# Performance work log

Hardware: AMD Instinct MI355X
Metric: run time of the kernel (lower is better)

The kernel has to match this reference:

```python
import jax, jax.numpy as jnp
import numpy as np

T, IN, HID, OUT, B = 256, 1024, 1024, 1024, 128


def setup_inputs() -> dict:
    key = jax.random.key(0)
    k1, k2, k3, k4 = jax.random.split(key, 4)
    return {
        "inputs": jax.random.normal(k1, (T, IN, B), dtype=jnp.float32),
        "h_prev": jnp.zeros((HID, B), dtype=jnp.float32),
        "Wxh": jax.random.normal(k2, (HID, IN), dtype=jnp.float32) * 0.01,
        "Whh": jax.random.normal(k3, (HID, HID), dtype=jnp.float32) * 0.01,
        "Why": jax.random.normal(k4, (OUT, HID), dtype=jnp.float32) * 0.01,
        "bh": jnp.zeros((HID, 1), dtype=jnp.float32),
        "by": jnp.zeros((OUT, 1), dtype=jnp.float32),
    }


def reference(inputs, h_prev, Wxh, Whh, Why, bh, by):
    # inputs: [T, IN, B]; h: [HID, B]
    def step(h, x):
        h = jnp.tanh(Wxh @ x + Whh @ h + bh)
        y = Why @ h + by
        return h, y

    h_final, ys = jax.lax.scan(step, h_prev, inputs)
    return ys, h_final  # ys: [T, OUT, B], h_final: [HID, B]
```

## Files before the change

kernel.cpp:

```cpp
#include <hip/hip_runtime.h>
#include <cmath>

#define T_STEPS 256
#define DIN  1024
#define DHID 1024
#define DOUT 1024
#define NB   128
#define BH   (DHID*NB)

typedef unsigned short u16;
typedef unsigned int   u32;
typedef unsigned long long u64;
typedef __attribute__((ext_vector_type(8))) __bf16 bf16x8;
typedef __attribute__((ext_vector_type(4))) float  f32x4;

__device__ __forceinline__ u16 f2bf(float f){
  u32 u = __builtin_bit_cast(u32, f);
  u32 r = (u + 0x7fffu + ((u >> 16) & 1u)) >> 16;
  return (u16)r;
}
__device__ __forceinline__ float bf2f(u16 h){
  u32 u = ((u32)h) << 16;
  return __builtin_bit_cast(float, u);
}

__device__ __forceinline__ u64 ld_agent_u64(const u64* p){
  return __hip_atomic_load(p, __ATOMIC_RELAXED, __HIP_MEMORY_SCOPE_AGENT);
}
__device__ __forceinline__ void st_agent_u64(u64* p, u64 v){
  __hip_atomic_store(p, v, __ATOMIC_RELAXED, __HIP_MEMORY_SCOPE_AGENT);
}

__global__ __launch_bounds__(256) void wconv(const float* __restrict__ w0,
                                             const float* __restrict__ w1,
                                             const float* __restrict__ w2,
                                             u16* __restrict__ dst){
  const int idx = blockIdx.x*256 + threadIdx.x;
  const int seg = idx >> 18;
  const int off = idx & 262143;
  const float* src = seg==0 ? w0 : (seg==1 ? w1 : w2);
  const float4 v = ((const float4*)src)[off];
  ushort4 o = make_ushort4(f2bf(v.x), f2bf(v.y), f2bf(v.z), f2bf(v.w));
  ((ushort4*)dst)[idx] = o;
}

__global__ __launch_bounds__(256) void hprevT(const float* __restrict__ hp,
                                              u16* __restrict__ HT0){
  const int tid = blockIdx.x*256 + threadIdx.x;
  const int b = tid >> 10, m = tid & 1023;
  HT0[tid] = f2bf(hp[(size_t)m*NB + b]);
}

__global__ __launch_bounds__(256) void xT_k(const float* __restrict__ x,
                                            u16* __restrict__ xt){
  __shared__ float tile[64][65];
  const int t  = blockIdx.z;
  const int k0 = blockIdx.y*64;
  const int b0 = blockIdx.x*64;
  const int tx = threadIdx.x & 63, ty = threadIdx.x >> 6;
  const float* src = x + (size_t)t*DIN*NB + (size_t)k0*NB + b0;
#pragma unroll
  for(int r=0;r<16;r++){ int k = r*4 + ty; tile[k][tx] = src[(size_t)k*NB + tx]; }
  __syncthreads();
  u16* dst = xt + (size_t)t*NB*DIN + (size_t)b0*DIN + k0;
#pragma unroll
  for(int r=0;r<16;r++){ int b = r*4 + ty; dst[(size_t)b*DIN + tx] = f2bf(tile[tx][b]); }
}

__global__ __launch_bounds__(256) void gemm_xw(const u16* __restrict__ XT,
                                               const u16* __restrict__ WxB,
                                               const float* __restrict__ bh,
                                               u16* __restrict__ AT){
  const int t  = blockIdx.y;
  const int mj = blockIdx.x;
  __shared__ __align__(16) u16 As[128*40];
  __shared__ __align__(16) u16 Bs[128*40];
  const u16* aG = XT + (size_t)t*NB*DIN;
  const u16* bG = WxB + (size_t)mj*128*DIN;
  const int tid = threadIdx.x;
  const int lane = tid & 63, w = tid >> 6;
  const int wr = (w & 1)*64, wc = (w >> 1)*64;
  const int l15 = lane & 15, q = lane >> 4;
  const int sr = tid >> 2;
  const int sk = (tid & 3)*8;

  f32x4 acc[4][4] = {};
  uint4 pa0 = *(const uint4*)&aG[(size_t)sr*DIN + sk];
  uint4 pa1 = *(const uint4*)&aG[(size_t)(sr+64)*DIN + sk];
  uint4 pb0 = *(const uint4*)&bG[(size_t)sr*DIN + sk];
  uint4 pb1 = *(const uint4*)&bG[(size_t)(sr+64)*DIN + sk];

  for(int it = 0; it < DIN/32; ++it){
    __syncthreads();
    *(uint4*)&As[sr*40 + sk]      = pa0;
    *(uint4*)&As[(sr+64)*40 + sk] = pa1;
    *(uint4*)&Bs[sr*40 + sk]      = pb0;
    *(uint4*)&Bs[(sr+64)*40 + sk] = pb1;
    __syncthreads();
    if(it < DIN/32 - 1){
      const int k0 = (it+1)*32;
      pa0 = *(const uint4*)&aG[(size_t)sr*DIN + k0 + sk];
      pa1 = *(const uint4*)&aG[(size_t)(sr+64)*DIN + k0 + sk];
      pb0 = *(const uint4*)&bG[(size_t)sr*DIN + k0 + sk];
      pb1 = *(const uint4*)&bG[(size_t)(sr+64)*DIN + k0 + sk];
    }
    bf16x8 af[4], bf[4];
#pragma unroll
    for(int i=0;i<4;i++) af[i] = *(const bf16x8*)&As[(wr + i*16 + l15)*40 + q*8];
#pragma unroll
    for(int j=0;j<4;j++) bf[j] = *(const bf16x8*)&Bs[(wc + j*16 + l15)*40 + q*8];
#pragma unroll
    for(int i=0;i<4;i++)
#pragma unroll
      for(int j=0;j<4;j++)
        acc[i][j] = __builtin_amdgcn_mfma_f32_16x16x32_bf16(af[i], bf[j], acc[i][j], 0,0,0);
  }

  u16* out = AT + (size_t)t*NB*DHID;
#pragma unroll
  for(int j=0;j<4;j++){
    const int mg = mj*128 + wc + j*16 + l15;
    const float bhv = bh[mg];
#pragma unroll
    for(int i=0;i<4;i++){
#pragma unroll
      for(int r=0;r<4;r++){
        const int bg = wr + i*16 + q*4 + r;
        out[(size_t)bg*DHID + mg] = f2bf(acc[i][j][r] + bhv);
      }
    }
  }
}

#define RSTEP_BLOCKS 64
__global__ __launch_bounds__(256, 1) void rnn_steps(const u16* __restrict__ WhB,
                                                    const u16* __restrict__ AT,
                                                    u16* __restrict__ HT,
                                                    u32* __restrict__ flags){
  const int mslice = blockIdx.x & 7;
  const int bg     = blockIdx.x >> 3;
  __shared__ __align__(16) u16 Hs[16*1032];
  __shared__ __align__(16) u16 Es[4*16*40];
  const int tid = threadIdx.x;
  const int lane = tid & 63, w = tid >> 6;
  const int l15 = lane & 15, q = lane >> 4, q8 = q*8;
  const int mw = mslice*128 + w*32;

  bf16x8 wf0[32], wf1[32];
  { const u16* ws0 = WhB + (size_t)(mw + l15)*DHID;
    const u16* ws1 = WhB + (size_t)(mw + 16 + l15)*DHID;
#pragma unroll
    for(int i=0;i<32;i++){ wf0[i] = *(const bf16x8*)&ws0[i*32 + q8];
                           wf1[i] = *(const bf16x8*)&ws1[i*32 + q8]; }
  }

  const int hr = tid >> 4;
  const int hc = tid & 15;
  const int eb = lane >> 2, ec = lane & 3;

  for(int t=0; t<T_STEPS; ++t){
    const u64* Hp64 = (const u64*)(HT + (size_t)t*BH + (size_t)(bg*16 + hr)*DHID) + hc;

    u64 hv[16];
#pragma unroll
    for(int i=0;i<16;i++) hv[i] = ld_agent_u64(Hp64 + i*16);

    const u16* At = AT + (size_t)t*BH;
    u16 aval[2][4];
#pragma unroll
    for(int h=0;h<2;h++)
#pragma unroll
      for(int r=0;r<4;r++)
        aval[h][r] = At[(size_t)(bg*16 + q*4 + r)*DHID + mw + h*16 + l15];

    u64* hs64 = (u64*)&Hs[hr*1032] + hc;
#pragma unroll
    for(int i=0;i<16;i++) hs64[i*16] = hv[i];
    __syncthreads();

    f32x4 a0e = {0,0,0,0}, a0o = {0,0,0,0}, a1e = {0,0,0,0}, a1o = {0,0,0,0};
#pragma unroll
    for(int kk=0;kk<32;kk+=2){
      bf16x8 ae = *(const bf16x8*)&Hs[l15*1032 + kk*32 + q8];
      bf16x8 ao = *(const bf16x8*)&Hs[l15*1032 + (kk+1)*32 + q8];
      a0e = __builtin_amdgcn_mfma_f32_16x16x32_bf16(ae, wf0[kk],   a0e, 0,0,0);
      a1e = __builtin_amdgcn_mfma_f32_16x16x32_bf16(ae, wf1[kk],   a1e, 0,0,0);
      a0o = __builtin_amdgcn_mfma_f32_16x16x32_bf16(ao, wf0[kk+1], a0o, 0,0,0);
      a1o = __builtin_amdgcn_mfma_f32_16x16x32_bf16(ao, wf1[kk+1], a1o, 0,0,0);
    }
    f32x4 acc0 = a0e + a0o, acc1 = a1e + a1o;

    u16* Ew = Es + w*640;
#pragma unroll
    for(int r=0;r<4;r++){
      float v0 = acc0[r] + bf2f(aval[0][r]);
      float v1 = acc1[r] + bf2f(aval[1][r]);
      Ew[(q*4+r)*40 + l15]      = f2bf(tanhf(v0));
      Ew[(q*4+r)*40 + 16 + l15] = f2bf(tanhf(v1));
    }
    __syncthreads();
    u64 h0 = *(const u64*)&Ew[eb*40 + ec*8];
    u64 h1 = *(const u64*)&Ew[eb*40 + ec*8 + 4];
    u64* Hn = (u64*)(HT + (size_t)(t+1)*BH + (size_t)(bg*16 + eb)*DHID + mw + ec*8);
    st_agent_u64(Hn,     h0);
    st_agent_u64(Hn + 1, h1);

    asm volatile("s_waitcnt vmcnt(0)" ::: "memory");

    if(t < T_STEPS-1){
      __syncthreads();
      if(tid == 0)
        __hip_atomic_store(&flags[(size_t)(bg*8 + mslice)*32], (u32)(t+1),
                           __ATOMIC_RELAXED, __HIP_MEMORY_SCOPE_AGENT);
      if(tid < 8){
        while(__hip_atomic_load(&flags[(size_t)(bg*8 + tid)*32],
                                __ATOMIC_RELAXED, __HIP_MEMORY_SCOPE_AGENT) < (u32)(t+1))
          ;
      }
      __syncthreads();
    }
  }
}

__global__ __launch_bounds__(256) void gemm_hy(const u16* __restrict__ WyB,
                                               const u16* __restrict__ HT,
                                               const float* __restrict__ by,
                                               float* __restrict__ Y){
  const int t  = blockIdx.y;
  const int mi = blockIdx.x;
  __shared__ __align__(16) u16 As[128*40];
  __shared__ __align__(16) u16 Bs[128*40];
  const u16* aG = WyB + (size_t)mi*128*DHID;
  const u16* bG = HT  + (size_t)(t+1)*BH;
  const int tid = threadIdx.x;
  const int lane = tid & 63, w = tid >> 6;
  const int wr = (w & 1)*64, wc = (w >> 1)*64;
  const int l15 = lane & 15, q = lane >> 4;
  const int sr = tid >> 2;
  const int sk = (tid & 3)*8;

  f32x4 acc[4][4] = {};
  uint4 pa0 = *(const uint4*)&aG[(size_t)sr*DHID + sk];
  uint4 pa1 = *(const uint4*)&aG[(size_t)(sr+64)*DHID + sk];
  uint4 pb0 = *(const uint4*)&bG[(size_t)sr*DHID + sk];
  uint4 pb1 = *(const uint4*)&bG[(size_t)(sr+64)*DHID + sk];

  for(int it = 0; it < DHID/32; ++it){
    __syncthreads();
    *(uint4*)&As[sr*40 + sk]      = pa0;
    *(uint4*)&As[(sr+64)*40 + sk] = pa1;
    *(uint4*)&Bs[sr*40 + sk]      = pb0;
    *(uint4*)&Bs[(sr+64)*40 + sk] = pb1;
    __syncthreads();
    if(it < DHID/32 - 1){
      const int k0 = (it+1)*32;
      pa0 = *(const uint4*)&aG[(size_t)sr*DHID + k0 + sk];
      pa1 = *(const uint4*)&aG[(size_t)(sr+64)*DHID + k0 + sk];
      pb0 = *(const uint4*)&bG[(size_t)sr*DHID + k0 + sk];
      pb1 = *(const uint4*)&bG[(size_t)(sr+64)*DHID + k0 + sk];
    }
    bf16x8 af[4], bf[4];
#pragma unroll
    for(int i=0;i<4;i++) af[i] = *(const bf16x8*)&As[(wr + i*16 + l15)*40 + q*8];
#pragma unroll
    for(int j=0;j<4;j++) bf[j] = *(const bf16x8*)&Bs[(wc + j*16 + l15)*40 + q*8];
#pragma unroll
    for(int i=0;i<4;i++)
#pragma unroll
      for(int j=0;j<4;j++)
        acc[i][j] = __builtin_amdgcn_mfma_f32_16x16x32_bf16(af[i], bf[j], acc[i][j], 0,0,0);
  }

  float* out = Y + (size_t)t*DOUT*NB;
#pragma unroll
  for(int i=0;i<4;i++){
#pragma unroll
    for(int r=0;r<4;r++){
      const int og = mi*128 + wr + i*16 + q*4 + r;
      const float byv = by[og];
#pragma unroll
      for(int j=0;j<4;j++){
        const int bg = wc + j*16 + l15;
        out[(size_t)og*NB + bg] = acc[i][j][r] + byv;
      }
    }
  }
}

__global__ __launch_bounds__(256) void hfinal(const u16* __restrict__ HT,
                                              float* __restrict__ dst){
  const int tid = blockIdx.x*256 + threadIdx.x;
  const int m = tid >> 7, b = tid & 127;
  dst[tid] = bf2f(HT[(size_t)T_STEPS*BH + (size_t)b*DHID + m]);
}

extern "C" void kernel_launch(void* const* d_in, const int* in_sizes, int n_in,
                              void* d_out, int out_size, void* d_ws, size_t ws_size,
                              hipStream_t stream)
{
  const float* x   = (const float*)d_in[0];
  const float* hp  = (const float*)d_in[1];
  const float* wxh = (const float*)d_in[2];
  const float* whh = (const float*)d_in[3];
  const float* why = (const float*)d_in[4];
  const float* bh  = (const float*)d_in[5];
  const float* by  = (const float*)d_in[6];
  float* out = (float*)d_out;

  u16* WxB = (u16*)d_ws;
  u16* WhB = WxB + (size_t)1024*1024;
  u16* WyB = WhB + (size_t)1024*1024;
  u16* HT  = WyB + (size_t)1024*1024;
  u32* flags = (u32*)(HT + (size_t)(T_STEPS+1)*BH);

  u16* XT = (u16*)d_out;
  u16* AT = XT + (size_t)T_STEPS*NB*DIN;

  wconv  <<<3072, 256, 0, stream>>>(wxh, whh, why, WxB);
  hprevT <<<512,  256, 0, stream>>>(hp, HT);
  xT_k   <<<dim3(2,16,T_STEPS), 256, 0, stream>>>(x, XT);
  gemm_xw<<<dim3(8,T_STEPS),    256, 0, stream>>>(XT, WxB, bh, AT);
  (void)hipMemsetAsync(flags, 0, 8192, stream);
  rnn_steps<<<RSTEP_BLOCKS, 256, 0, stream>>>(WhB, AT, HT, flags);
  gemm_hy<<<dim3(8,T_STEPS), 256, 0, stream>>>(WyB, HT, by, out);
  hfinal <<<512, 256, 0, stream>>>(HT, out + (size_t)T_STEPS*DOUT*NB);
}
```

Baseline: 1.446 ms.

## Restructure recurrent step sync: per-wave spin, direct-to-LDS H loads, prefetch inputs

The recurrent kernel now has every wave spin on its own dependency flag at the top of each step, replacing the tid<8 spin followed by a barrier. The previous hidden state is loaded straight into LDS with global_load_lds instead of going through registers, and the next step's input-projection values are prefetched right after the flag is published. A workgroup-wide barrier is replaced by a block fence before the per-wave epilogue reads. This is meant to shorten the serial per-step critical path, at the cost of subtler memory-ordering assumptions: relaxed flag loads followed by direct-to-LDS loads, and only a wave-local fence on the Es reads.

```diff
diff --git a/kernel.cpp b/kernel.cpp
--- a/kernel.cpp
+++ b/kernel.cpp
@@ -24,11 +24,16 @@
   return __builtin_bit_cast(float, u);
 }
 
-__device__ __forceinline__ u64 ld_agent_u64(const u64* p){
+__device__ __forceinline__ u32 ld_agent_u32(const u32* p){
   return __hip_atomic_load(p, __ATOMIC_RELAXED, __HIP_MEMORY_SCOPE_AGENT);
 }
 __device__ __forceinline__ void st_agent_u64(u64* p, u64 v){
   __hip_atomic_store(p, v, __ATOMIC_RELAXED, __HIP_MEMORY_SCOPE_AGENT);
+}
+__device__ __forceinline__ void gload_lds16(const void* g, void* l){
+  __builtin_amdgcn_global_load_lds(
+      (const __attribute__((address_space(1))) unsigned int*)g,
+      (__attribute__((address_space(3))) unsigned int*)l, 16, 0, 0);
 }
 
 __global__ __launch_bounds__(256) void wconv(const float* __restrict__ w0,
@@ -154,28 +159,31 @@
                            wf1[i] = *(const bf16x8*)&ws1[i*32 + q8]; }
   }
 
-  const int hr = tid >> 4;
-  const int hc = tid & 15;
   const int eb = lane >> 2, ec = lane & 3;
+  const u32* fl = &flags[(size_t)(bg*8 + (lane & 7))*32];
+
+  u16 avn[2][4];
+#pragma unroll
+  for(int h=0;h<2;h++)
+#pragma unroll
+    for(int r=0;r<4;r++)
+      avn[h][r] = AT[(size_t)(bg*16 + q*4 + r)*DHID + mw + h*16 + l15];
 
   for(int t=0; t<T_STEPS; ++t){
-    const u64* Hp64 = (const u64*)(HT + (size_t)t*BH + (size_t)(bg*16 + hr)*DHID) + hc;
-
-    u64 hv[16];
-#pragma unroll
-    for(int i=0;i<16;i++) hv[i] = ld_agent_u64(Hp64 + i*16);
-
-    const u16* At = AT + (size_t)t*BH;
-    u16 aval[2][4];
-#pragma unroll
-    for(int h=0;h<2;h++)
-#pragma unroll
-      for(int r=0;r<4;r++)
-        aval[h][r] = At[(size_t)(bg*16 + q*4 + r)*DHID + mw + h*16 + l15];
-
-    u64* hs64 = (u64*)&Hs[hr*1032] + hc;
-#pragma unroll
-    for(int i=0;i<16;i++) hs64[i*16] = hv[i];
+    while(ld_agent_u32(fl) < (u32)t)
+      ;
+
+    { const u16* hbase = HT + (size_t)t*BH + (size_t)(bg*16)*DHID;
+#pragma unroll
+      for(int i=0;i<4;i++){
+        const int row = w*4 + i;
+#pragma unroll
+        for(int half=0; half<2; half++){
+          const u16* gp = hbase + (size_t)row*DHID + half*512 + lane*8;
+          gload_lds16(gp, &Hs[row*1032 + half*512]);
+        }
+      }
+    }
     __syncthreads();
 
     f32x4 a0e = {0,0,0,0}, a0o = {0,0,0,0}, a1e = {0,0,0,0}, a1o = {0,0,0,0};
@@ -193,12 +201,12 @@
     u16* Ew = Es + w*640;
 #pragma unroll
     for(int r=0;r<4;r++){
-      float v0 = acc0[r] + bf2f(aval[0][r]);
-      float v1 = acc1[r] + bf2f(aval[1][r]);
+      float v0 = acc0[r] + bf2f(avn[0][r]);
+      float v1 = acc1[r] + bf2f(avn[1][r]);
       Ew[(q*4+r)*40 + l15]      = f2bf(tanhf(v0));
       Ew[(q*4+r)*40 + 16 + l15] = f2bf(tanhf(v1));
     }
-    __syncthreads();
+    __threadfence_block();
     u64 h0 = *(const u64*)&Ew[eb*40 + ec*8];
     u64 h1 = *(const u64*)&Ew[eb*40 + ec*8 + 4];
     u64* Hn = (u64*)(HT + (size_t)(t+1)*BH + (size_t)(bg*16 + eb)*DHID + mw + ec*8);
@@ -206,18 +214,18 @@
     st_agent_u64(Hn + 1, h1);
 
     asm volatile("s_waitcnt vmcnt(0)" ::: "memory");
+    __syncthreads();
 
     if(t < T_STEPS-1){
-      __syncthreads();
       if(tid == 0)
         __hip_atomic_store(&flags[(size_t)(bg*8 + mslice)*32], (u32)(t+1),
                            __ATOMIC_RELAXED, __HIP_MEMORY_SCOPE_AGENT);
-      if(tid < 8){
-        while(__hip_atomic_load(&flags[(size_t)(bg*8 + tid)*32],
-                                __ATOMIC_RELAXED, __HIP_MEMORY_SCOPE_AGENT) < (u32)(t+1))
-          ;
-      }
-      __syncthreads();
+      const u16* At = AT + (size_t)(t+1)*BH;
+#pragma unroll
+      for(int h=0;h<2;h++)
+#pragma unroll
+        for(int r=0;r<4;r++)
+          avn[h][r] = At[(size_t)(bg*16 + q*4 + r)*DHID + mw + h*16 + l15];
     }
   }
 }
```

Result: no change. 1.426 ms (-1.4%).
